# Performance work log

Measured on AMD Instinct MI355X. Metric: run time of the kernel, lower is better.

Reference implementation:

```python
import jax, jax.numpy as jnp
import numpy as np

B_, L_, C_ = 4, 2048, 384
EXPAND, H_, N_ = 2, 12, 64
DI = EXPAND * C_          # 768 d_inner
DH = DI // H_             # 64 head dim
HID = 4 * C_              # 1536 mlp hidden
EPS = 1e-5


def layernorm(x, g, b):
    mu = jnp.mean(x, -1, keepdims=True)
    var = jnp.mean((x - mu) ** 2, -1, keepdims=True)
    return (x - mu) * jax.lax.rsqrt(var + EPS) * g + b


def ssm_dir(x, Win, bin_, dtb, Alog, D, Wout, bout):
    """Multihead (Mamba2-style) selective scan. x:(B,L,C) -> (B,L,C)."""
    B, L, _ = x.shape
    zxbcdt = x @ Win + bin_  # (B,L, 2*DI+2*N+H)
    z = zxbcdt[..., :DI]
    xs = zxbcdt[..., DI:2 * DI].reshape(B, L, H_, DH)
    Bt = zxbcdt[..., 2 * DI:2 * DI + N_]
    Ct = zxbcdt[..., 2 * DI + N_:2 * DI + 2 * N_]
    dt = jax.nn.softplus(zxbcdt[..., 2 * DI + 2 * N_:] + dtb)  # (B,L,H)
    A = -jnp.exp(Alog)  # (H,)

    def step(h, inp):
        x_t, B_t, C_t, dt_t = inp  # (B,H,DH),(B,N),(B,N),(B,H)
        a = jnp.exp(dt_t * A)  # (B,H)
        h = a[..., None, None] * h + (dt_t[..., None] * x_t)[..., None] * B_t[:, None, None, :]
        y = jnp.einsum('bhdn,bn->bhd', h, C_t)
        return h, y

    h0 = jnp.zeros((B, H_, DH, N_), x.dtype)
    xsT = jnp.moveaxis(xs, 1, 0)
    _, ys = jax.lax.scan(step, h0, (xsT, jnp.moveaxis(Bt, 1, 0), jnp.moveaxis(Ct, 1, 0), jnp.moveaxis(dt, 1, 0)))
    y = jnp.moveaxis(ys, 0, 1) + D.reshape(H_, DH) * xs  # (B,L,H,DH)
    y = y.reshape(B, L, DI) * jax.nn.silu(z)
    return y @ Wout + bout


def reference(points, g1, be1, g2, be2,
              Winf, binf, dtbf, Alogf, Df, Woutf, boutf,
              Winb, binb, dtbb, Alogb, Db, Woutb, boutb,
              W1, b1m, bng, bnb, W2, b2m):
    # --- token mixer (Parallel bidirectional SSM), pre-norm residual ---
    shortcut = points
    x = layernorm(points, g1, be1)
    fwd = ssm_dir(x, Winf, binf, dtbf, Alogf, Df, Woutf, boutf)
    bwd = jnp.flip(ssm_dir(jnp.flip(x, -2), Winb, binb, dtbb, Alogb, Db, Woutb, boutb), -2)
    x = fwd + bwd + shortcut
    # --- channel mixer (Conv1d k=1 == dense), BatchNorm in eval mode ---
    shortcut = x
    h = layernorm(x, g2, be2)
    h = h @ W1.T + b1m  # (B,L,HID)
    h = (h * (bng / np.sqrt(1.0 + EPS))) + bnb  # BN eval, running mean 0 var 1
    h = jax.nn.relu(h)
    h = h @ W2.T + b2m
    return h + shortcut


def setup_inputs() -> dict:
    key = jax.random.key(0)
    ks = jax.random.split(key, 32)
    s = 0.02
    PROJ = 2 * DI + 2 * N_ + H_

    def dir_params(i):
        return dict(
            Win=jax.random.normal(ks[i], (C_, PROJ)) * s,
            bin_=jnp.zeros((PROJ,)),
            dtb=jnp.log(jnp.expm1(jax.random.uniform(ks[i + 1], (H_,), minval=0.001, maxval=0.1))),
            Alog=jnp.log(jnp.arange(1, H_ + 1, dtype=jnp.float32)),
            D=jnp.ones((DI,)),
            Wout=jax.random.normal(ks[i + 2], (DI, C_)) * s,
            bout=jnp.zeros((C_,)))

    f, b = dir_params(1), dir_params(4)
    return {
        'points': jax.random.normal(ks[0], (B_, L_, C_)),
        'g1': jnp.ones((C_,)), 'be1': jnp.zeros((C_,)),
        'g2': jnp.ones((C_,)), 'be2': jnp.zeros((C_,)),
        'Winf': f['Win'], 'binf': f['bin_'], 'dtbf': f['dtb'], 'Alogf': f['Alog'], 'Df': f['D'], 'Woutf': f['Wout'], 'boutf': f['bout'],
        'Winb': b['Win'], 'binb': b['bin_'], 'dtbb': b['dtb'], 'Alogb': b['Alog'], 'Db': b['D'], 'Woutb': b['Wout'], 'boutb': b['bout'],
        'W1': jax.random.normal(ks[7], (HID, C_)) * s, 'b1m': jnp.zeros((HID,)),
        'bng': jnp.ones((HID,)), 'bnb': jnp.zeros((HID,)),
        'W2': jax.random.normal(ks[8], (C_, HID)) * s, 'b2m': jnp.zeros((C_,)),
    }
```

## Files before the change

kernel.cpp:

```cpp
#include <hip/hip_runtime.h>
#include <hip/hip_bf16.h>

typedef unsigned short u16;
typedef unsigned int   u32;

#define DEVINL static __device__ __forceinline__

constexpr int Bb   = 4;
constexpr int Ll   = 2048;
constexpr int Cc   = 384;
constexpr int Hh   = 12;
constexpr int Nn   = 64;
constexpr int DHh  = 64;
constexpr int DIi  = 768;
constexpr int PROJ = 2*DIi + 2*Nn + Hh;
constexpr int PROJp= 1792;
constexpr int ZROW = 2*PROJp;
constexpr int HIDh = 1536;
constexpr int TOK  = Bb*Ll;

constexpr int NWINP  = PROJp*Cc;
constexpr int NWOUTC = Cc*2*DIi;
constexpr int NW1    = HIDh*Cc;
constexpr int NW2    = Cc*HIDh;

typedef __attribute__((ext_vector_type(8))) short bf16x8;
typedef __attribute__((ext_vector_type(4))) float f32x4;

DEVINL float u2f(u32 u){ union { u32 i; float f; } c; c.i = u << 16; return c.f; }
DEVINL u16 f2u(float f){
  u32 x = __float_as_uint(f);
  x += 0x7fffu + ((x >> 16) & 1u);
  return (u16)(x >> 16);
}
DEVINL bf16x8 lds_ld8(const u16* p){
  union { uint2 q[2]; bf16x8 v; } r;
  r.q[0] = *reinterpret_cast<const uint2*>(p);
  r.q[1] = *reinterpret_cast<const uint2*>(p + 4);
  return r.v;
}
DEVINL float ing(const void* p, size_t i, bool f32){
  return f32 ? ((const float*)p)[i] : u2f(((const u16*)p)[i]);
}
DEVINL float softplusf(float v){
  if (v > 20.f) return v;
  return log1pf(expf(v));
}
DEVINL float sigmoidf(float z){
  if (z >= 0.f) { return 1.f / (1.f + expf(-z)); }
  float e = expf(z);
  return e / (1.f + e);
}
DEVINL bool is_f32(const u32* g1w){ return g1w[0] == 0x3F800000u; }

DEVINL void gload16(const u16* g, u16* l){
  __builtin_amdgcn_global_load_lds(
      (const __attribute__((address_space(1))) void*)g,
      (__attribute__((address_space(3))) void*)l, 16, 0, 0);
}

DEVINL int xcd_swz2d(){
  int nwg = gridDim.x * gridDim.y;
  int bid = blockIdx.y * gridDim.x + blockIdx.x;
  int qc = nwg >> 3, rc = nwg & 7;
  int xcd = bid & 7, loc = bid >> 3;
  return (xcd < rc) ? (xcd*(qc+1) + loc) : (rc*(qc+1) + (xcd-rc)*qc + loc);
}
DEVINL void xcd_cyb(int& c, int& yy, int& b8){
  int ny = gridDim.y, nz = gridDim.z;
  int nwg = gridDim.x * ny * nz;
  int lid = (blockIdx.z*ny + blockIdx.y)*gridDim.x + blockIdx.x;
  int qc = nwg >> 3, rc = nwg & 7;
  int xcd = lid & 7, loc = lid >> 3;
  int swz = (xcd < rc) ? (xcd*(qc+1) + loc) : (rc*(qc+1) + (xcd-rc)*qc + loc);
  yy = swz % ny;
  int t = swz / ny;
  b8 = t % nz;
  c = t / nz;
}

__global__ __launch_bounds__(256) void wtr_kernel(
    const void* __restrict__ s0, const void* __restrict__ s1,
    const void* __restrict__ s2, const void* __restrict__ s3,
    const void* __restrict__ s4, const void* __restrict__ s5,
    u16* __restrict__ wt, const u32* __restrict__ flg)
{
  __shared__ u16 t[32][33];
  bool f32 = is_f32(flg);
  int z = blockIdx.z;
  if (z == 4){
    u16* dst = wt + 2*NWINP + NWOUTC;
    for (int i = blockIdx.x*256 + threadIdx.x; i < NW1 + NW2; i += gridDim.x*256){
      const void* src = (i < NW1) ? s4 : s5;
      int off = (i < NW1) ? i : i - NW1;
      dst[i] = f32 ? f2u(((const float*)src)[off]) : ((const u16*)src)[off];
    }
    return;
  }
  const void* src = (z==0)? s0 : (z==1)? s1 : (z==2)? s2 : s3;
  const int R    = (z<2)? Cc   : DIi;
  const int Csrc = (z<2)? PROJ : Cc;
  const int Np   = (z<2)? PROJp: Cc;
  const int dstr = (z<2)? Cc   : 2*DIi;
  const int doff = (z==3)? DIi : 0;
  u16* dst = wt + ((z==0)? 0 : (z==1)? NWINP : 2*NWINP);
  int tilesx = Np/32, tilesy = R/32;
  int tid = blockIdx.x;
  if (tid >= tilesx*tilesy) return;
  int n0 = (tid % tilesx)*32, k0 = (tid / tilesx)*32;
  int tx = threadIdx.x & 31, ty = threadIdx.x >> 5;
  #pragma unroll
  for (int rr=0; rr<32; rr+=8){
    int k = k0+ty+rr, n = n0+tx;
    float v = (n < Csrc) ? ing(src, (size_t)k*Csrc + n, f32) : 0.f;
    t[ty+rr][tx] = f2u(v);
  }
  __syncthreads();
  #pragma unroll
  for (int rr=0; rr<32; rr+=8){
    int n = n0+ty+rr, k = k0+tx;
    dst[(size_t)n*dstr + doff + k] = t[tx][ty+rr];
  }
}

template<int MODE>
__global__ __launch_bounds__(256) void ln_kernel(
    const void* __restrict__ in, const void* __restrict__ g,
    const void* __restrict__ be, u16* __restrict__ out, const u32* __restrict__ flg)
{
  bool f32 = is_f32(flg);
  int tok  = blockIdx.x*4 + (threadIdx.x >> 6);
  int lane = threadIdx.x & 63;
  size_t base = (size_t)tok * Cc;
  float v[6];
  #pragma unroll
  for (int j=0;j<6;j++){
    size_t idx = base + lane + 64*j;
    v[j] = (MODE == 1) ? ((const float*)in)[idx] : ing(in, idx, f32);
  }
  float s = 0.f;
  #pragma unroll
  for (int j=0;j<6;j++) s += v[j];
  #pragma unroll
  for (int o=32;o;o>>=1) s += __shfl_xor(s, o, 64);
  float mu = s * (1.0f/Cc);
  float q = 0.f;
  #pragma unroll
  for (int j=0;j<6;j++){ float d = v[j]-mu; q = fmaf(d,d,q); }
  #pragma unroll
  for (int o=32;o;o>>=1) q += __shfl_xor(q, o, 64);
  float rs = rsqrtf(q*(1.0f/Cc) + 1e-5f);
  #pragma unroll
  for (int j=0;j<6;j++){
    int c = lane + 64*j;
    out[base + c] = f2u((v[j]-mu)*rs*ing(g, c, f32) + ing(be, c, f32));
  }
}

template<int EPI, int BM, int BN>
__global__ __launch_bounds__(256) void mgemm_kernel(
    const u16* __restrict__ A, const u16* __restrict__ A2, int KA,
    const u16* __restrict__ Bm,
    int M, int N, int K, int lda,
    const void* __restrict__ bias, const void* __restrict__ bng,
    const void* __restrict__ bnb,  const void* __restrict__ resb, size_t res_off,
    const float* resf, u16* __restrict__ outb, float* outf, void* outv,
    const u32* __restrict__ flg)
{
  constexpr int BK = 32;
  constexpr int WR = (BM == 128) ? 2 : 4;
  constexpr int WC = 4 / WR;
  constexpr int RH = BM / WR;
  constexpr int CW = BN / WC;
  constexpr int SM = RH / 16;
  constexpr int SN = CW / 16;

  bool f32 = is_f32(flg);
  __shared__ u16 As[BM*BK] __attribute__((aligned(16)));
  __shared__ u16 Bs[BN*BK] __attribute__((aligned(16)));
  const int tid  = threadIdx.x;
  const int lane = tid & 63;
  const int w    = tid >> 6;
  const int q    = lane >> 4;
  const int r16  = lane & 15;
  const int wr   = (WC == 1) ? w : (w >> 1);
  const int wc   = (WC == 1) ? 0 : (w & 1);
  const int swz = xcd_swz2d();
  const int m0 = (swz / gridDim.x) * BM, n0 = (swz % gridDim.x) * BN;

  f32x4 acc[SM][SN] = {};

  const int srow = lane >> 2;
  const int sgl  = lane & 3;

  for (int k0 = 0; k0 < K; k0 += BK) {
    const u16* Ab = A; int kc0 = k0;
    if (KA && k0 >= KA){ Ab = A2; kc0 = k0 - KA; }
    #pragma unroll
    for (int j = 0; j < BM/64; j++){
      int r0  = (w*(BM/64) + j)*16;
      int row = r0 + srow;
      int gl  = sgl ^ (row & 3);
      gload16(Ab + (size_t)(m0+row)*lda + kc0 + gl*8, &As[r0*BK]);
    }
    #pragma unroll
    for (int j = 0; j < BN/64; j++){
      int r0  = (w*(BN/64) + j)*16;
      int row = r0 + srow;
      int gl  = sgl ^ (row & 3);
      gload16(Bm + (size_t)(n0+row)*K + k0 + gl*8, &Bs[r0*BK]);
    }
    __syncthreads();
    bf16x8 af[SM], bfr[SN];
    #pragma unroll
    for (int i=0;i<SM;i++){
      int ar = wr*RH + i*16 + r16;
      af[i] = *reinterpret_cast<const bf16x8*>(&As[ar*BK + ((q ^ (ar&3)) << 3)]);
    }
    #pragma unroll
    for (int s=0;s<SN;s++){
      int br = wc*CW + s*16 + r16;
      bfr[s] = *reinterpret_cast<const bf16x8*>(&Bs[br*BK + ((q ^ (br&3)) << 3)]);
    }
    #pragma unroll
    for (int i=0;i<SM;i++)
      #pragma unroll
      for (int s=0;s<SN;s++)
        acc[i][s] = __builtin_amdgcn_mfma_f32_16x16x32_bf16(af[i], bfr[s], acc[i][s], 0,0,0);
    __syncthreads();
  }

  const float RSQ = 0.9999950000374997f;
  #pragma unroll
  for (int i=0;i<SM;i++){
    #pragma unroll
    for (int s=0;s<SN;s++){
      int gcol = n0 + wc*CW + s*16 + r16;
      if (gcol >= N) continue;
      #pragma unroll
      for (int rr=0;rr<4;rr++){
        int grow = m0 + wr*RH + i*16 + q*4 + rr;
        size_t o = (size_t)grow*N + gcol;
        float v = acc[i][s][rr];
        if constexpr (EPI == 0) {
          outb[o] = f2u(v + ing(bias, gcol, f32));
        } else if constexpr (EPI == 5) {
          int cc = gcol;
          const void* bp = bias;
          if (cc >= PROJp) { cc -= PROJp; bp = bng; }
          if (cc > PROJ-1) cc = PROJ-1;
          outb[o] = f2u(v + ing(bp, cc, f32));
        } else if constexpr (EPI == 1) {
          outf[o] = v + ing(bias, gcol, f32) + ing(bng, gcol, f32)
                      + ing(resb, res_off + o, f32);
        } else if constexpr (EPI == 2) {
          float t = (v + ing(bias, gcol, f32)) * (ing(bng, gcol, f32) * RSQ) + ing(bnb, gcol, f32);
          outb[o] = f2u(t > 0.f ? t : 0.f);
        } else {
          float t = v + ing(bias, gcol, f32) + resf[o];
          if (f32) ((float*)outv)[o] = t; else ((u16*)outv)[o] = f2u(t);
        }
      }
    }
  }
}


__global__ __launch_bounds__(256) void scan_state_kernel(
    const u16* __restrict__ zx, const void* __restrict__ dtb0,
    const void* __restrict__ dtb1, const void* __restrict__ Alog0,
    const void* __restrict__ Alog1, u16* __restrict__ states,
    float* __restrict__ P, int QQ, const u32* __restrict__ flg)
{
  bool f32 = is_f32(flg);
  int c, h, b8;
  xcd_cyb(c, h, b8);
  int dir = b8 >> 2, b = b8 & 3;
  int zoff = dir * PROJp;
  int NC = gridDim.x;
  int lane = threadIdx.x & 63;
  int d0   = (threadIdx.x >> 6) * 16;
  float hst[16];
  #pragma unroll
  for (int j=0;j<16;j++) hst[j] = 0.f;
  float Af = -expf(ing(dir ? Alog1 : Alog0, h, f32));
  float dtbh = ing(dir ? dtb1 : dtb0, h, f32);
  float p = 1.f;
  for (int i=0;i<QQ;i++){
    int tl = c*QQ + i;
    int t  = dir ? (Ll-1-tl) : tl;
    size_t row = ((size_t)b*Ll + t) * ZROW + zoff;
    float dt = softplusf(u2f(zx[row + 2*DIi + 2*Nn + h]) + dtbh);
    float a  = expf(fmaxf(dt*Af, -80.f));
    float u  = dt * u2f(zx[row + 2*DIi + lane]);
    const u16* xrow = zx + row + DIi + h*DHh + d0;
    #pragma unroll
    for (int j=0;j<16;j++) hst[j] = a*hst[j] + u*u2f(xrow[j]);
    p *= a;
  }
  int g = ((dir*Bb + b)*Hh + h)*NC + c;
  u16* sp = states + (size_t)g*4096;
  #pragma unroll
  for (int j=0;j<16;j++) sp[(d0+j)*64 + lane] = f2u(hst[j]);
  if (threadIdx.x == 0) P[g] = p;
}

__global__ __launch_bounds__(256) void scan_state32m4_kernel(
    const u16* __restrict__ zx, const void* __restrict__ dtb0,
    const void* __restrict__ dtb1, const void* __restrict__ Alog0,
    const void* __restrict__ Alog1, u16* __restrict__ states,
    float* __restrict__ P, const u32* __restrict__ flg)
{
  constexpr int Q = 32;
  __shared__ u16 Braw[Q][68];
  __shared__ u16 XT[4][64][36];
  __shared__ u16 BwT[4][64][36];
  __shared__ float wv4[4][Q];
  bool f32 = is_f32(flg);
  int c, hg, b8;
  xcd_cyb(c, hg, b8);
  int dir = b8 >> 2, b = b8 & 3;
  int zoff = dir * PROJp;
  int NC = gridDim.x;
  int tid = threadIdx.x;
  int w = tid >> 6, lane = tid & 63;
  int h = hg*4 + w;
  int q = lane >> 4, r16 = lane & 15;
  int g = ((dir*Bb + b)*Hh + h)*NC + c;
  float Af = -expf(ing(dir ? Alog1 : Alog0, h, f32));
  float dtbh = ing(dir ? dtb1 : dtb0, h, f32);

  {
    int i = tid >> 3, p = tid & 7;
    int tl = c*Q + i;
    int t  = dir ? (Ll-1-tl) : tl;
    const u16* sb = zx + ((size_t)b*Ll + t)*ZROW + zoff + 2*DIi + p*8;
    uint2 b0 = *reinterpret_cast<const uint2*>(sb);
    uint2 b1 = *reinterpret_cast<const uint2*>(sb + 4);
    *reinterpret_cast<uint2*>(&Braw[i][p*8])   = b0;
    *reinterpret_cast<uint2*>(&Braw[i][p*8+4]) = b1;
  }
  #pragma unroll
  for (int rep=0; rep<4; rep++){
    int j = rep*64 + lane;
    int i = j >> 3, p = j & 7;
    int tl = c*Q + i;
    int t  = dir ? (Ll-1-tl) : tl;
    const u16* sx = zx + ((size_t)b*Ll + t)*ZROW + zoff + DIi + h*DHh + p*8;
    uint2 a0 = *reinterpret_cast<const uint2*>(sx);
    uint2 a1 = *reinterpret_cast<const uint2*>(sx + 4);
    u16 tmp[8];
    *reinterpret_cast<uint2*>(&tmp[0]) = a0;
    *reinterpret_cast<uint2*>(&tmp[4]) = a1;
    #pragma unroll
    for (int e=0;e<8;e++) XT[w][p*8+e][i] = tmp[e];
  }
  float dt, la;
  {
    int tl = c*Q + (lane & 31);
    int t  = dir ? (Ll-1-tl) : tl;
    float draw = u2f(zx[((size_t)b*Ll + t)*ZROW + zoff + 2*DIi + 2*Nn + h]);
    dt = softplusf(draw + dtbh);
    la = fmaxf(dt*Af, -80.f);
  }
  float L = la;
  #pragma unroll
  for (int off=1; off<32; off<<=1){
    float tv = __shfl_up(L, off, 32);
    if ((lane & 31) >= off) L += tv;
  }
  float Lt = __shfl(L, 31, 32);
  if (lane < Q) wv4[w][lane] = expf(fmaxf(Lt - L, -80.f)) * dt;
  if (lane == 0) P[g] = expf(fmaxf(Lt, -87.f));
  __syncthreads();
  #pragma unroll
  for (int rep=0; rep<4; rep++){
    int j = rep*64 + lane;
    int i = j >> 3, p = j & 7;
    float wsc = wv4[w][i];
    u16 tmp[8];
    *reinterpret_cast<uint2*>(&tmp[0]) = *reinterpret_cast<const uint2*>(&Braw[i][p*8]);
    *reinterpret_cast<uint2*>(&tmp[4]) = *reinterpret_cast<const uint2*>(&Braw[i][p*8+4]);
    #pragma unroll
    for (int e=0;e<8;e++) BwT[w][p*8+e][i] = f2u(wsc * u2f(tmp[e]));
  }
  __syncthreads();

  f32x4 acc[4][4] = {};
  bf16x8 af[4];
  #pragma unroll
  for (int mt=0;mt<4;mt++) af[mt] = lds_ld8(&XT[w][mt*16+r16][q*8]);
  #pragma unroll
  for (int nt=0;nt<4;nt++){
    bf16x8 bf = lds_ld8(&BwT[w][nt*16+r16][q*8]);
    #pragma unroll
    for (int mt=0;mt<4;mt++)
      acc[mt][nt] = __builtin_amdgcn_mfma_f32_16x16x32_bf16(af[mt], bf, acc[mt][nt], 0,0,0);
  }
  u16* sp = states + (size_t)g*4096;
  #pragma unroll
  for (int mt=0;mt<4;mt++)
    #pragma unroll
    for (int nt=0;nt<4;nt++)
      #pragma unroll
      for (int rr=0;rr<4;rr++){
        int d = mt*16 + q*4 + rr, n = nt*16 + r16;
        sp[d*64 + n] = f2u(acc[mt][nt][rr]);
      }
}

template<int NC>
__global__ __launch_bounds__(256) void scan_combine_kernel(
    u16* __restrict__ states, const float* __restrict__ P)
{
  __shared__ float ps[(NC > 64) ? NC : 64];
  int g   = blockIdx.x >> 4;
  int idx = ((blockIdx.x & 15) << 8) | threadIdx.x;
  if (threadIdx.x < NC) ps[threadIdx.x] = P[g*NC + threadIdx.x];
  __syncthreads();
  size_t base = (size_t)g*NC*4096 + idx;
  float sv[NC];
  #pragma unroll
  for (int c=0;c<NC;c++) sv[c] = u2f(states[base + (size_t)c*4096]);
  float hr = 0.f;
  #pragma unroll
  for (int c=0;c<NC;c++){
    states[base + (size_t)c*4096] = f2u(hr);
    hr = ps[c]*hr + sv[c];
  }
}

__global__ __launch_bounds__(64) void scan_out_kernel(
    const u16* __restrict__ zx, const void* __restrict__ dtb0,
    const void* __restrict__ dtb1, const void* __restrict__ Alog0,
    const void* __restrict__ Alog1, const void* __restrict__ D0,
    const void* __restrict__ D1, const u16* __restrict__ hinit,
    u16* __restrict__ ych0, int QQ, const u32* __restrict__ flg)
{
  bool f32 = is_f32(flg);
  int c, h, b8;
  xcd_cyb(c, h, b8);
  int dir = b8 >> 2, b = b8 & 3;
  int zoff = dir * PROJp;
  int NC = gridDim.x;
  int lane = threadIdx.x;
  int g = ((dir*Bb + b)*Hh + h)*NC + c;
  u16* ych = ych0 + (size_t)dir*((size_t)TOK*DIi);
  float hs[64];
  const u16* hp = hinit + (size_t)g*4096 + lane*64;
  #pragma unroll
  for (int n=0;n<64;n++) hs[n] = u2f(hp[n]);
  float Af = -expf(ing(dir ? Alog1 : Alog0, h, f32));
  float dtbh = ing(dir ? dtb1 : dtb0, h, f32);
  float Dv = ing(dir ? D1 : D0, h*DHh + lane, f32);
  for (int i=0;i<QQ;i++){
    int tl = c*QQ + i;
    int t  = dir ? (Ll-1-tl) : tl;
    size_t row = ((size_t)b*Ll + t) * ZROW + zoff;
    float dt = softplusf(u2f(zx[row + 2*DIi + 2*Nn + h]) + dtbh);
    float a  = expf(fmaxf(dt*Af, -80.f));
    float xv = u2f(zx[row + DIi + h*DHh + lane]);
    float zv = u2f(zx[row + h*DHh + lane]);
    const u16* Brow = zx + row + 2*DIi;
    const u16* Crow = Brow + Nn;
    float u = dt * xv;
    float y0=0.f, y1=0.f, y2=0.f, y3=0.f;
    #pragma unroll
    for (int j=0;j<16;j++){
      float h0 = a*hs[j]    + u*u2f(Brow[j]);    hs[j]   =h0; y0 = fmaf(h0, u2f(Crow[j]),    y0);
      float h1 = a*hs[j+16] + u*u2f(Brow[j+16]); hs[j+16]=h1; y1 = fmaf(h1, u2f(Crow[j+16]), y1);
      float h2 = a*hs[j+32] + u*u2f(Brow[j+32]); hs[j+32]=h2; y2 = fmaf(h2, u2f(Crow[j+32]), y2);
      float h3 = a*hs[j+48] + u*u2f(Brow[j+48]); hs[j+48]=h3; y3 = fmaf(h3, u2f(Crow[j+48]), y3);
    }
    float y = (y0+y1)+(y2+y3);
    float yo = y + Dv*xv;
    float sg = zv * sigmoidf(zv);
    ych[((size_t)(b*Ll + t))*DIi + h*DHh + lane] = f2u(yo * sg);
  }
}

__global__ __launch_bounds__(256) void scan_out32m4_kernel(
    const u16* __restrict__ zx, const void* __restrict__ dtb0,
    const void* __restrict__ dtb1, const void* __restrict__ Alog0,
    const void* __restrict__ Alog1, const void* __restrict__ D0,
    const void* __restrict__ D1, const u16* __restrict__ hinit,
    u16* __restrict__ ych0, const u32* __restrict__ flg)
{
  constexpr int Q = 32;
  __shared__ u16 bc[Q][132];
  __shared__ u16 XT[4][64][36];
  __shared__ u16 gp[4][Q][36];
  __shared__ float Lss[4][Q], dts[4][Q];
  bool f32 = is_f32(flg);
  int c, hg, b8;
  xcd_cyb(c, hg, b8);
  int dir = b8 >> 2, b = b8 & 3;
  int zoff = dir * PROJp;
  int NC = gridDim.x;
  int tid = threadIdx.x;
  int w = tid >> 6, lane = tid & 63;
  int h = hg*4 + w;
  int q = lane >> 4, r16 = lane & 15;
  int g = ((dir*Bb + b)*Hh + h)*NC + c;
  u16* ych = ych0 + (size_t)dir*((size_t)TOK*DIi);
  float Af = -expf(ing(dir ? Alog1 : Alog0, h, f32));
  float dtbh = ing(dir ? dtb1 : dtb0, h, f32);

  #pragma unroll
  for (int rep=0; rep<2; rep++){
    int j = rep*256 + tid;
    int i = j >> 4, p = j & 15;
    int tl = c*Q + i;
    int t  = dir ? (Ll-1-tl) : tl;
    const u16* sb = zx + ((size_t)b*Ll + t)*ZROW + zoff + 2*DIi + p*8;
    uint2 b0 = *reinterpret_cast<const uint2*>(sb);
    uint2 b1 = *reinterpret_cast<const uint2*>(sb + 4);
    *reinterpret_cast<uint2*>(&bc[i][p*8])   = b0;
    *reinterpret_cast<uint2*>(&bc[i][p*8+4]) = b1;
  }
  #pragma unroll
  for (int rep=0; rep<4; rep++){
    int j = rep*64 + lane;
    int i = j >> 3, p = j & 7;
    int tl = c*Q + i;
    int t  = dir ? (Ll-1-tl) : tl;
    const u16* sx = zx + ((size_t)b*Ll + t)*ZROW + zoff + DIi + h*DHh + p*8;
    uint2 a0 = *reinterpret_cast<const uint2*>(sx);
    uint2 a1 = *reinterpret_cast<const uint2*>(sx + 4);
    u16 tmp[8];
    *reinterpret_cast<uint2*>(&tmp[0]) = a0;
    *reinterpret_cast<uint2*>(&tmp[4]) = a1;
    #pragma unroll
    for (int e=0;e<8;e++) XT[w][p*8+e][i] = tmp[e];
  }
  float dt, la;
  {
    int tl = c*Q + (lane & 31);
    int t  = dir ? (Ll-1-tl) : tl;
    float draw = u2f(zx[((size_t)b*Ll + t)*ZROW + zoff + 2*DIi + 2*Nn + h]);
    dt = softplusf(draw + dtbh);
    la = fmaxf(dt*Af, -80.f);
  }
  float L = la;
  #pragma unroll
  for (int off=1; off<32; off<<=1){
    float tv = __shfl_up(L, off, 32);
    if ((lane & 31) >= off) L += tv;
  }
  if (lane < Q){ Lss[w][lane] = L; dts[w][lane] = dt; }
  __syncthreads();

  f32x4 gacc[2][2] = {};
  #pragma unroll
  for (int kk=0; kk<2; kk++){
    bf16x8 ac[2], bb[2];
    #pragma unroll
    for (int mt=0;mt<2;mt++) ac[mt] = lds_ld8(&bc[mt*16+r16][64 + kk*32 + q*8]);
    #pragma unroll
    for (int nt=0;nt<2;nt++) bb[nt] = lds_ld8(&bc[nt*16+r16][kk*32 + q*8]);
    #pragma unroll
    for (int mt=0;mt<2;mt++)
      #pragma unroll
      for (int nt=0;nt<2;nt++)
        gacc[mt][nt] = __builtin_amdgcn_mfma_f32_16x16x32_bf16(ac[mt], bb[nt], gacc[mt][nt], 0,0,0);
  }
  float iL[2][4], sL[2], sdt[2];
  #pragma unroll
  for (int mt=0;mt<2;mt++)
    #pragma unroll
    for (int rr=0;rr<4;rr++) iL[mt][rr] = Lss[w][mt*16 + q*4 + rr];
  #pragma unroll
  for (int nt=0;nt<2;nt++){ int s = nt*16 + r16; sL[nt] = Lss[w][s]; sdt[nt] = dts[w][s]; }
  #pragma unroll
  for (int mt=0;mt<2;mt++)
    #pragma unroll
    for (int nt=0;nt<2;nt++)
      #pragma unroll
      for (int rr=0;rr<4;rr++){
        int i = mt*16 + q*4 + rr, s = nt*16 + r16;
        float m = (i >= s) ? expf(fmaxf(iL[mt][rr]-sL[nt], -80.f))*sdt[nt] : 0.f;
        gp[w][i][s] = f2u(gacc[mt][nt][rr] * m);
      }
  __syncthreads();

  f32x4 aI[2][4] = {}, aS[2][4] = {};
  {
    bf16x8 ag[2];
    #pragma unroll
    for (int mt=0;mt<2;mt++) ag[mt] = lds_ld8(&gp[w][mt*16+r16][q*8]);
    #pragma unroll
    for (int nt=0;nt<4;nt++){
      bf16x8 bx = lds_ld8(&XT[w][nt*16+r16][q*8]);
      #pragma unroll
      for (int mt=0;mt<2;mt++)
        aI[mt][nt] = __builtin_amdgcn_mfma_f32_16x16x32_bf16(ag[mt], bx, aI[mt][nt], 0,0,0);
    }
  }
  #pragma unroll
  for (int kk=0; kk<2; kk++){
    bf16x8 ac[2];
    #pragma unroll
    for (int mt=0;mt<2;mt++) ac[mt] = lds_ld8(&bc[mt*16+r16][64 + kk*32 + q*8]);
    #pragma unroll
    for (int nt=0;nt<4;nt++){
      const u16* hp = hinit + (size_t)g*4096 + (nt*16+r16)*64 + kk*32 + q*8;
      bf16x8 bh = *reinterpret_cast<const bf16x8*>(hp);
      #pragma unroll
      for (int mt=0;mt<2;mt++)
        aS[mt][nt] = __builtin_amdgcn_mfma_f32_16x16x32_bf16(ac[mt], bh, aS[mt][nt], 0,0,0);
    }
  }

  float Dv[4];
  #pragma unroll
  for (int nt=0;nt<4;nt++) Dv[nt] = ing(dir ? D1 : D0, h*DHh + nt*16 + r16, f32);
  #pragma unroll
  for (int mt=0;mt<2;mt++)
    #pragma unroll
    for (int rr=0;rr<4;rr++){
      int i = mt*16 + q*4 + rr;
      float ei = expf(fmaxf(iL[mt][rr], -87.f));
      int tl = c*Q + i;
      int t  = dir ? (Ll-1-tl) : tl;
      size_t rowz = ((size_t)b*Ll + t)*ZROW + zoff + (size_t)h*DHh;
      size_t obase = ((size_t)(b*Ll + t))*DIi + h*DHh;
      #pragma unroll
      for (int nt=0;nt<4;nt++){
        int d = nt*16 + r16;
        float xv = u2f(XT[w][d][i]);
        float zv = u2f(zx[rowz + d]);
        float y  = aI[mt][nt][rr] + ei*aS[mt][nt][rr] + Dv[nt]*xv;
        ych[obase + d] = f2u(y * zv * sigmoidf(zv));
      }
    }
}

extern "C" void kernel_launch(void* const* d_in, const int* in_sizes, int n_in,
                              void* d_out, int out_size, void* d_ws, size_t ws_size,
                              hipStream_t stream)
{
  (void)in_sizes; (void)n_in; (void)out_size;
  const void* points = d_in[0];
  const void* g1   = d_in[1];
  const void* be1  = d_in[2];
  const void* g2   = d_in[3];
  const void* be2  = d_in[4];
  const void* Win[2]  = { d_in[5],  d_in[12] };
  const void* bin[2]  = { d_in[6],  d_in[13] };
  const void* dtb[2]  = { d_in[7],  d_in[14] };
  const void* Alog[2] = { d_in[8],  d_in[15] };
  const void* Dd[2]   = { d_in[9],  d_in[16] };
  const void* Wout[2] = { d_in[10], d_in[17] };
  const void* bout[2] = { d_in[11], d_in[18] };
  const void* W1   = d_in[19];
  const void* b1m  = d_in[20];
  const void* bng  = d_in[21];
  const void* bnb  = d_in[22];
  const void* W2   = d_in[23];
  const void* b2m  = d_in[24];
  const u32* g1w = (const u32*)g1;

  auto align256 = [](size_t x){ return (x + 255) & ~(size_t)255; };
  constexpr size_t ZXB  = (size_t)TOK*ZROW*2;
  constexpr size_t YCHB = (size_t)TOK*DIi*2;
  constexpr size_t MLPB = (size_t)TOK*HIDh*2;
  constexpr size_t XB   = (size_t)TOK*Cc*2;
  constexpr size_t X1B  = (size_t)TOK*Cc*4;
  constexpr size_t WTB  = ((size_t)2*NWINP + NWOUTC + NW1 + NW2) * 2;

  auto scan_bytes = [&](int NCc)->size_t {
    size_t STBc = (size_t)2*Bb*Hh*NCc*4096*2;
    size_t PBc  = align256((size_t)2*Bb*Hh*NCc*4);
    return ZXB + 2*YCHB + STBc + PBc + 4096;
  };
  auto need_for = [&](int NCc)->size_t {
    size_t scan = scan_bytes(NCc);
    size_t RBc  = scan > MLPB ? scan : MLPB;
    return 256 + align256(XB) + align256(RBc) + align256(X1B) + align256(WTB) + 4096;
  };
  int NCr = 8;
  if (need_for(16) <= ws_size) NCr = 16;
  if (need_for(32) <= ws_size) NCr = 32;
  if (need_for(64) <= ws_size) NCr = 64;
  const int QQr = Ll / NCr;
  const size_t STB = (size_t)2*Bb*Hh*NCr*4096*2;
  const size_t SCAN = scan_bytes(NCr);
  const size_t RB = SCAN > MLPB ? SCAN : MLPB;

  char* ws = (char*)d_ws;
  size_t off = 0;
  auto alloc = [&](size_t bytes) -> char* {
    char* p = ws + off;
    off += align256(bytes);
    return p;
  };
  u16*   x    = (u16*)  alloc(XB);
  char*  Rbig =         alloc(RB);
  float* x1   = (float*)alloc(X1B);
  u16*   wt   = (u16*)  alloc(WTB);
  u16*   zx     = (u16*)Rbig;
  u16*   ych0   = (u16*)(Rbig + ZXB);
  u16*   ych1   = (u16*)(Rbig + ZXB + YCHB);
  u16*   states = (u16*)(Rbig + ZXB + 2*YCHB);
  float* P      = (float*)(Rbig + ZXB + 2*YCHB + STB);
  u16*   hin2   = x;
  u16*   hmid   = (u16*)Rbig;
  u16* WinTT    = wt;
  u16* WoutTT   = wt + 2*NWINP;
  u16* W1b      = wt + 2*NWINP + NWOUTC;
  u16* W2b      = W1b + NW1;
  (void)ych1; (void)W2b;

  wtr_kernel<<<dim3(672,1,5), 256, 0, stream>>>(
      Win[0], Win[1], Wout[0], Wout[1], W1, W2, wt, g1w);

  ln_kernel<0><<<TOK/4, 256, 0, stream>>>(points, g1, be1, x, g1w);

  mgemm_kernel<5,128,128><<<dim3(ZROW/128, TOK/128), 256, 0, stream>>>(
      x, nullptr, 0, WinTT, TOK, ZROW, Cc, Cc, bin[0],
      bin[1], nullptr, nullptr, 0, nullptr, zx, nullptr, nullptr, g1w);

  if (QQr == 32) {
    scan_state32m4_kernel<<<dim3(NCr, Hh/4, 2*Bb), 256, 0, stream>>>(
        zx, dtb[0], dtb[1], Alog[0], Alog[1], states, P, g1w);
  } else {
    scan_state_kernel<<<dim3(NCr, Hh, 2*Bb), 256, 0, stream>>>(
        zx, dtb[0], dtb[1], Alog[0], Alog[1], states, P, QQr, g1w);
  }
  if (NCr == 64)      scan_combine_kernel<64><<<2*Bb*Hh*16, 256, 0, stream>>>(states, P);
  else if (NCr == 32) scan_combine_kernel<32><<<2*Bb*Hh*16, 256, 0, stream>>>(states, P);
  else if (NCr == 16) scan_combine_kernel<16><<<2*Bb*Hh*16, 256, 0, stream>>>(states, P);
  else                scan_combine_kernel< 8><<<2*Bb*Hh*16, 256, 0, stream>>>(states, P);
  if (QQr == 32) {
    scan_out32m4_kernel<<<dim3(NCr, Hh/4, 2*Bb), 256, 0, stream>>>(
        zx, dtb[0], dtb[1], Alog[0], Alog[1], Dd[0], Dd[1], states, ych0, g1w);
  } else {
    scan_out_kernel<<<dim3(NCr, Hh, 2*Bb), 64, 0, stream>>>(
        zx, dtb[0], dtb[1], Alog[0], Alog[1], Dd[0], Dd[1], states, ych0, QQr, g1w);
  }

  mgemm_kernel<1,128,64><<<dim3(Cc/64, TOK/128), 256, 0, stream>>>(
      ych0, ych0 + (size_t)TOK*DIi, DIi, WoutTT, TOK, Cc, 2*DIi, DIi, bout[0],
      bout[1], nullptr, points, 0, nullptr,
      nullptr, x1, nullptr, g1w);

  ln_kernel<1><<<TOK/4, 256, 0, stream>>>(x1, g2, be2, hin2, g1w);

  mgemm_kernel<2,128,128><<<dim3(HIDh/128, TOK/128), 256, 0, stream>>>(
      hin2, nullptr, 0, W1b, TOK, HIDh, Cc, Cc, b1m,
      bng, bnb, nullptr, 0, nullptr, hmid, nullptr, nullptr, g1w);

  mgemm_kernel<3,128,64><<<dim3(Cc/64, TOK/128), 256, 0, stream>>>(
      hmid, nullptr, 0, W1b + NW1, TOK, Cc, HIDh, HIDh, b2m,
      nullptr, nullptr, nullptr, 0, x1, nullptr, nullptr, d_out, g1w);
}
```

Baseline: 381.4 us.

## Double GEMM K-tile to 64 and stage bf16 epilogue through LDS

Raises the GEMM K-step from 32 to 64 with an 8-way XOR swizzle, halving the number of barrier-separated iterations per tile. For the EPI 5 and EPI 2 epilogues, results are first written to a shared LDS buffer that reuses the A/B staging space, then stored to global memory as coalesced 16-byte rows instead of scattered 2-byte stores. The cost is more LDS per block, which may lower occupancy. The staged path also drops the gcol<N bounds check, so it assumes N is a multiple of BN.

New measurement: 339.9 us. -10.9%, faster.

```diff
diff --git a/kernel.cpp b/kernel.cpp
--- a/kernel.cpp
+++ b/kernel.cpp
@@ -167,17 +167,19 @@
     const float* resf, u16* __restrict__ outb, float* outf, void* outv,
     const u32* __restrict__ flg)
 {
-  constexpr int BK = 32;
+  constexpr int BK = 64;
   constexpr int WR = (BM == 128) ? 2 : 4;
   constexpr int WC = 4 / WR;
   constexpr int RH = BM / WR;
   constexpr int CW = BN / WC;
   constexpr int SM = RH / 16;
   constexpr int SN = CW / 16;
+  constexpr int LDSZ = (BM*BK + BN*BK) > (BM*BN) ? (BM*BK + BN*BK) : (BM*BN);
 
   bool f32 = is_f32(flg);
-  __shared__ u16 As[BM*BK] __attribute__((aligned(16)));
-  __shared__ u16 Bs[BN*BK] __attribute__((aligned(16)));
+  __shared__ u16 smem[LDSZ] __attribute__((aligned(16)));
+  u16* As = smem;
+  u16* Bs = smem + BM*BK;
   const int tid  = threadIdx.x;
   const int lane = tid & 63;
   const int w    = tid >> 6;
@@ -190,47 +192,89 @@
 
   f32x4 acc[SM][SN] = {};
 
-  const int srow = lane >> 2;
-  const int sgl  = lane & 3;
+  const int srow = lane >> 3;
+  const int sgl  = lane & 7;
 
   for (int k0 = 0; k0 < K; k0 += BK) {
     const u16* Ab = A; int kc0 = k0;
     if (KA && k0 >= KA){ Ab = A2; kc0 = k0 - KA; }
     #pragma unroll
-    for (int j = 0; j < BM/64; j++){
-      int r0  = (w*(BM/64) + j)*16;
+    for (int j = 0; j < BM/32; j++){
+      int r0  = (w*(BM/32) + j)*8;
       int row = r0 + srow;
-      int gl  = sgl ^ (row & 3);
+      int gl  = sgl ^ (row & 7);
       gload16(Ab + (size_t)(m0+row)*lda + kc0 + gl*8, &As[r0*BK]);
     }
     #pragma unroll
-    for (int j = 0; j < BN/64; j++){
-      int r0  = (w*(BN/64) + j)*16;
+    for (int j = 0; j < BN/32; j++){
+      int r0  = (w*(BN/32) + j)*8;
       int row = r0 + srow;
-      int gl  = sgl ^ (row & 3);
+      int gl  = sgl ^ (row & 7);
       gload16(Bm + (size_t)(n0+row)*K + k0 + gl*8, &Bs[r0*BK]);
     }
     __syncthreads();
-    bf16x8 af[SM], bfr[SN];
+    #pragma unroll
+    for (int kk = 0; kk < 2; kk++){
+      bf16x8 af[SM], bfr[SN];
+      #pragma unroll
+      for (int i=0;i<SM;i++){
+        int ar = wr*RH + i*16 + r16;
+        af[i] = *reinterpret_cast<const bf16x8*>(&As[ar*BK + (((kk*4+q) ^ (ar&7)) << 3)]);
+      }
+      #pragma unroll
+      for (int s=0;s<SN;s++){
+        int br = wc*CW + s*16 + r16;
+        bfr[s] = *reinterpret_cast<const bf16x8*>(&Bs[br*BK + (((kk*4+q) ^ (br&7)) << 3)]);
+      }
+      #pragma unroll
+      for (int i=0;i<SM;i++)
+        #pragma unroll
+        for (int s=0;s<SN;s++)
+          acc[i][s] = __builtin_amdgcn_mfma_f32_16x16x32_bf16(af[i], bfr[s], acc[i][s], 0,0,0);
+    }
+    __syncthreads();
+  }
+
+  const float RSQ = 0.9999950000374997f;
+  if constexpr (EPI == 5 || EPI == 2) {
     #pragma unroll
     for (int i=0;i<SM;i++){
-      int ar = wr*RH + i*16 + r16;
-      af[i] = *reinterpret_cast<const bf16x8*>(&As[ar*BK + ((q ^ (ar&3)) << 3)]);
-    }
-    #pragma unroll
-    for (int s=0;s<SN;s++){
-      int br = wc*CW + s*16 + r16;
-      bfr[s] = *reinterpret_cast<const bf16x8*>(&Bs[br*BK + ((q ^ (br&3)) << 3)]);
-    }
-    #pragma unroll
-    for (int i=0;i<SM;i++)
-      #pragma unroll
-      for (int s=0;s<SN;s++)
-        acc[i][s] = __builtin_amdgcn_mfma_f32_16x16x32_bf16(af[i], bfr[s], acc[i][s], 0,0,0);
+      #pragma unroll
+      for (int s=0;s<SN;s++){
+        int lcol = wc*CW + s*16 + r16;
+        int gcol = n0 + lcol;
+        #pragma unroll
+        for (int rr=0;rr<4;rr++){
+          int lrow = wr*RH + i*16 + q*4 + rr;
+          float v = acc[i][s][rr];
+          float t;
+          if constexpr (EPI == 5) {
+            int cc = gcol;
+            const void* bp = bias;
+            if (cc >= PROJp) { cc -= PROJp; bp = bng; }
+            if (cc > PROJ-1) cc = PROJ-1;
+            t = v + ing(bp, cc, f32);
+          } else {
+            t = (v + ing(bias, gcol, f32)) * (ing(bng, gcol, f32) * RSQ) + ing(bnb, gcol, f32);
+            t = t > 0.f ? t : 0.f;
+          }
+          smem[lrow*BN + lcol] = f2u(t);
+        }
+      }
+    }
     __syncthreads();
-  }
-
-  const float RSQ = 0.9999950000374997f;
+    constexpr int LPR = BN/8;
+    constexpr int RPP = 256/LPR;
+    const int erow = tid / LPR;
+    const int ecol = (tid % LPR)*8;
+    #pragma unroll
+    for (int pass=0; pass<BM/RPP; pass++){
+      int row = pass*RPP + erow;
+      *reinterpret_cast<uint4*>(&outb[(size_t)(m0+row)*N + n0 + ecol]) =
+        *reinterpret_cast<const uint4*>(&smem[row*BN + ecol]);
+    }
+    return;
+  }
   #pragma unroll
   for (int i=0;i<SM;i++){
     #pragma unroll
@@ -244,18 +288,9 @@
         float v = acc[i][s][rr];
         if constexpr (EPI == 0) {
           outb[o] = f2u(v + ing(bias, gcol, f32));
-        } else if constexpr (EPI == 5) {
-          int cc = gcol;
-          const void* bp = bias;
-          if (cc >= PROJp) { cc -= PROJp; bp = bng; }
-          if (cc > PROJ-1) cc = PROJ-1;
-          outb[o] = f2u(v + ing(bp, cc, f32));
         } else if constexpr (EPI == 1) {
           outf[o] = v + ing(bias, gcol, f32) + ing(bng, gcol, f32)
                       + ing(resb, res_off + o, f32);
-        } else if constexpr (EPI == 2) {
-          float t = (v + ing(bias, gcol, f32)) * (ing(bng, gcol, f32) * RSQ) + ing(bnb, gcol, f32);
-          outb[o] = f2u(t > 0.f ? t : 0.f);
         } else {
           float t = v + ing(bias, gcol, f32) + resf[o];
           if (f32) ((float*)outv)[o] = t; else ((u16*)outv)[o] = f2u(t);
```
